# Optimization experiments

Hardware: AMD Instinct MI355X
Metric: run time of the kernel (lower is better)

The kernel has to match this reference:

```python
import jax, jax.numpy as jnp
import numpy as np

N_ATOMS = 60000
N_BONDS = 150000
MAX_NB = 6
N_MOLS = 2000
ATOM_FDIM = 133
BOND_FDIM = 14
HID = 300
DEPTH = 3
TAB = 16
FFN_HID = 300
FFN_IN = HID * 2 + TAB  # 616


def setup_inputs() -> dict:
    key = jax.random.key(0)
    ks = iter(jax.random.split(key, 40))
    d = {}
    for c in ("il", "hl"):
        d[f"f_atoms_{c}"] = jax.random.normal(next(ks), (N_ATOMS, ATOM_FDIM), jnp.float32)
        d[f"f_bonds_{c}"] = jax.random.normal(next(ks), (N_BONDS, BOND_FDIM), jnp.float32)
        d[f"a2b_{c}"] = jax.random.randint(next(ks), (N_ATOMS, MAX_NB), 0, N_BONDS, jnp.int32)
        d[f"b2a_{c}"] = jax.random.randint(next(ks), (N_BONDS,), 0, N_ATOMS, jnp.int32)
        d[f"b2revb_{c}"] = jax.random.randint(next(ks), (N_BONDS,), 0, N_BONDS, jnp.int32)
        d[f"mol_ids_{c}"] = jnp.sort(jax.random.randint(next(ks), (N_ATOMS,), 0, N_MOLS, jnp.int32))
        d[f"W_i_{c}"] = jax.random.normal(next(ks), (ATOM_FDIM + BOND_FDIM, HID), jnp.float32) * 0.05
        d[f"W_h_{c}"] = jax.random.normal(next(ks), (HID, HID), jnp.float32) * 0.05
        d[f"W_o_w_{c}"] = jax.random.normal(next(ks), (ATOM_FDIM + HID, HID), jnp.float32) * 0.05
        d[f"W_o_b_{c}"] = jax.random.normal(next(ks), (HID,), jnp.float32) * 0.05
    d["tabular"] = jax.random.normal(next(ks), (N_MOLS, TAB), jnp.float32)
    d["ffn_w1"] = jax.random.normal(next(ks), (FFN_IN, FFN_HID), jnp.float32) * 0.05
    d["ffn_b1"] = jax.random.normal(next(ks), (FFN_HID,), jnp.float32) * 0.05
    d["ffn_w2"] = jax.random.normal(next(ks), (FFN_HID, FFN_HID), jnp.float32) * 0.05
    d["ffn_b2"] = jax.random.normal(next(ks), (FFN_HID,), jnp.float32) * 0.05
    d["head_w"] = jax.random.normal(next(ks), (FFN_HID, 1), jnp.float32) * 0.05
    d["head_b"] = jax.random.normal(next(ks), (1,), jnp.float32) * 0.05
    return d


def _encode(f_atoms, f_bonds, a2b, b2a, b2revb, mol_ids, W_i, W_h, W_o_w, W_o_b):
    relu = jax.nn.relu
    # message init from [src atom feats, bond feats]
    msg = relu(jnp.concatenate([f_atoms[b2a], f_bonds], axis=1) @ W_i)  # [n_bonds, H]

    def step(m, _):
        nei = m[a2b].sum(axis=1)          # [n_atoms, H] gather-sum over incoming bonds
        nm = nei[b2a] - m[b2revb]         # exclude reverse bond
        return relu(nm @ W_h), None

    msg, _ = jax.lax.scan(step, msg, None, length=DEPTH - 1)
    a_msg = msg[a2b].sum(axis=1)          # [n_atoms, H]
    atom_h = relu(jnp.concatenate([f_atoms, a_msg], axis=1) @ W_o_w + W_o_b)
    sums = jax.ops.segment_sum(atom_h, mol_ids, num_segments=N_MOLS)
    cnt = jax.ops.segment_sum(jnp.ones((atom_h.shape[0],), atom_h.dtype), mol_ids, num_segments=N_MOLS)
    return sums / jnp.maximum(cnt, 1.0)[:, None]  # mean; zeros if empty mol


def reference(f_atoms_il, f_bonds_il, a2b_il, b2a_il, b2revb_il, mol_ids_il,
              W_i_il, W_h_il, W_o_w_il, W_o_b_il,
              f_atoms_hl, f_bonds_hl, a2b_hl, b2a_hl, b2revb_hl, mol_ids_hl,
              W_i_hl, W_h_hl, W_o_w_hl, W_o_b_hl,
              tabular, ffn_w1, ffn_b1, ffn_w2, ffn_b2, head_w, head_b):
    mv_il = _encode(f_atoms_il, f_bonds_il, a2b_il, b2a_il, b2revb_il, mol_ids_il,
                    W_i_il, W_h_il, W_o_w_il, W_o_b_il)
    mv_hl = _encode(f_atoms_hl, f_bonds_hl, a2b_hl, b2a_hl, b2revb_hl, mol_ids_hl,
                    W_i_hl, W_h_hl, W_o_w_hl, W_o_b_hl)
    combined = jnp.concatenate([mv_il, mv_hl, tabular], axis=1)  # [n_mols, 616]
    h = jax.nn.relu(combined @ ffn_w1 + ffn_b1)
    fp = jax.nn.relu(h @ ffn_w2 + ffn_b2)
    return fp @ head_w + head_b  # [n_mols, 1]
```

## Files before the change

kernel.cpp:

```cpp
#include <hip/hip_runtime.h>
#include <hip/hip_bf16.h>

#define N_ATOMS 60000
#define N_BONDS 150000
#define MAX_NB 6
#define N_MOLS 2000
#define ATOM_FDIM 133
#define BOND_FDIM 14
#define HID 300
#define TAB 16

typedef __hip_bfloat16 bf16;
typedef __attribute__((ext_vector_type(8))) short short8;
typedef __attribute__((ext_vector_type(4))) float f32x4;

__device__ __forceinline__ float b2f(short s) {
  return __uint_as_float(((unsigned int)(unsigned short)s) << 16);
}
__device__ __forceinline__ short f2b(float f) {
  bf16 h = __float2bfloat16(f);
  return __builtin_bit_cast(short, h);
}

__device__ __forceinline__ float ldv(const float* __restrict__ p, size_t i) { return p[i]; }
__device__ __forceinline__ float ldv(const bf16* __restrict__ p, size_t i) { return __bfloat162float(p[i]); }
__device__ __forceinline__ void stv(float* __restrict__ p, size_t i, float v) { p[i] = v; }
__device__ __forceinline__ void stv(bf16* __restrict__ p, size_t i, float v) { p[i] = __float2bfloat16(v); }


template<int AMODE>
__device__ __forceinline__ short8 fetchA(int row, int kg,
                                         const bf16* __restrict__ src0,
                                         const bf16* __restrict__ src1,
                                         const int* __restrict__ gidx) {
  if constexpr (AMODE == 0) {
    return *(const short8*)(src0 + (size_t)row * 320 + kg * 8);
  } else if constexpr (AMODE == 1) {
    if (kg < 18) {
      const int a = gidx[row];
      return *(const short8*)(src0 + (size_t)a * 144 + kg * 8);
    } else {
      return *(const short8*)(src1 + (size_t)row * 16 + (kg - 18) * 8);
    }
  } else {
    if (kg < 18) return *(const short8*)(src0 + (size_t)row * 144 + kg * 8);
    else if (kg < 58) return *(const short8*)(src1 + (size_t)row * 320 + (kg - 18) * 8);
    else { short8 z = {}; return z; }
  }
}

template<int AMODE, typename TO, int KSTEPS>
__global__ __launch_bounds__(256)
void mfma_gemm(const bf16* __restrict__ src0, const bf16* __restrict__ src1,
               const int* __restrict__ gidx, const bf16* __restrict__ Wt,
               const float* __restrict__ bias, TO* __restrict__ C,
               int M, int Ncols, int ostride) {
  __shared__ __align__(16) short As[128 * 32];
  __shared__ __align__(16) short Bs[64 * 32];
  const int t = threadIdx.x;
  const int bm = blockIdx.x * 128;
  const int bn = blockIdx.y * 64;
  const int w = t >> 6, lane = t & 63;
  const int wr = w >> 1, wc = w & 1;
  const int lr = lane & 15, lk = lane >> 4;
  f32x4 acc[4][2] = {};
  for (int kt = 0; kt < KSTEPS; ++kt) {
    #pragma unroll
    for (int i = 0; i < 2; ++i) {
      const int s = t + 256 * i;
      const int row = s >> 2, kgl = s & 3;
      const int grow = bm + row;
      short8 v = {};
      if (grow < M) v = fetchA<AMODE>(grow, kt * 4 + kgl, src0, src1, gidx);
      *(short8*)(As + row * 32 + ((kgl ^ (row & 3)) << 3)) = v;
    }
    {
      const int col = t >> 2, kgl = t & 3;
      short8 v = *(const short8*)(Wt + (size_t)(bn + col) * (KSTEPS * 32) + (size_t)(kt * 4 + kgl) * 8);
      *(short8*)(Bs + col * 32 + ((kgl ^ (col & 3)) << 3)) = v;
    }
    __syncthreads();
    short8 afr[4], bfr[2];
    #pragma unroll
    for (int m = 0; m < 4; ++m) {
      const int r = wr * 64 + m * 16 + lr;
      afr[m] = *(const short8*)(As + r * 32 + ((lk ^ (r & 3)) << 3));
    }
    #pragma unroll
    for (int n = 0; n < 2; ++n) {
      const int cc = wc * 32 + n * 16 + lr;
      bfr[n] = *(const short8*)(Bs + cc * 32 + ((lk ^ (cc & 3)) << 3));
    }
    #pragma unroll
    for (int m = 0; m < 4; ++m)
      #pragma unroll
      for (int n = 0; n < 2; ++n)
        acc[m][n] = __builtin_amdgcn_mfma_f32_16x16x32_bf16(afr[m], bfr[n], acc[m][n], 0, 0, 0);
    __syncthreads();
  }
  #pragma unroll
  for (int m = 0; m < 4; ++m) {
    #pragma unroll
    for (int n = 0; n < 2; ++n) {
      #pragma unroll
      for (int r = 0; r < 4; ++r) {
        const int row = bm + wr * 64 + m * 16 + lk * 4 + r;
        const int col = bn + wc * 32 + n * 16 + lr;
        if (row >= M) continue;
        if (col < Ncols) {
          float v = acc[m][n][r];
          if (bias) v += bias[col];
          stv(C, (size_t)row * ostride + col, fmaxf(v, 0.f));
        } else if (col < ostride) {
          stv(C, (size_t)row * ostride + col, 0.f);
        }
      }
    }
  }
}

__global__ __launch_bounds__(256)
void cvt_pad_kernel(const float* __restrict__ src, bf16* __restrict__ dst,
                    int rows, int scols, int dcols) {
  const int i = blockIdx.x * blockDim.x + threadIdx.x;
  if (i >= rows * dcols) return;
  const int r = i / dcols, c = i % dcols;
  dst[(size_t)r * dcols + c] = __float2bfloat16(c < scols ? src[(size_t)r * scols + c] : 0.f);
}

__global__ __launch_bounds__(256)
void wt_fill_kernel(const float* __restrict__ W, bf16* __restrict__ Wt,
                    int N, int Kp, int seg0_len, int seg1_dst, int seg1_src, int seg1_len) {
  const int i = blockIdx.x * blockDim.x + threadIdx.x;
  if (i >= 320 * Kp) return;
  const int n = i / Kp, kd = i % Kp;
  float v = 0.f;
  if (n < N) {
    if (kd < seg0_len) v = W[(size_t)kd * N + n];
    else if (kd >= seg1_dst && kd < seg1_dst + seg1_len)
      v = W[(size_t)(seg1_src + kd - seg1_dst) * N + n];
  }
  Wt[(size_t)n * Kp + kd] = __float2bfloat16(v);
}

__global__ __launch_bounds__(256)
void nei_sum16_kernel(const bf16* __restrict__ msg, const int* __restrict__ a2b,
                      bf16* __restrict__ nei) {
  const int i = blockIdx.x * blockDim.x + threadIdx.x;
  if (i >= N_ATOMS * 40) return;
  const int a = i / 40, c8 = (i % 40) * 8;
  const int* ab = a2b + (size_t)a * MAX_NB;
  float s[8] = {};
  #pragma unroll
  for (int j = 0; j < MAX_NB; ++j) {
    short8 v = *(const short8*)(msg + (size_t)ab[j] * 320 + c8);
    #pragma unroll
    for (int e = 0; e < 8; ++e) s[e] += b2f(v[e]);
  }
  short8 o;
  #pragma unroll
  for (int e = 0; e < 8; ++e) o[e] = f2b(s[e]);
  *(short8*)(nei + (size_t)a * 320 + c8) = o;
}

__global__ __launch_bounds__(256)
void nm16_kernel(const bf16* __restrict__ nei, const bf16* __restrict__ msg,
                 const int* __restrict__ b2a, const int* __restrict__ b2revb,
                 bf16* __restrict__ nm) {
  const int i = blockIdx.x * blockDim.x + threadIdx.x;
  if (i >= N_BONDS * 40) return;
  const int e = i / 40, c8 = (i % 40) * 8;
  const int a = b2a[e], r = b2revb[e];
  short8 u = *(const short8*)(nei + (size_t)a * 320 + c8);
  short8 v = *(const short8*)(msg + (size_t)r * 320 + c8);
  short8 o;
  #pragma unroll
  for (int k = 0; k < 8; ++k) o[k] = f2b(b2f(u[k]) - b2f(v[k]));
  *(short8*)(nm + (size_t)e * 320 + c8) = o;
}

template<int MODE, typename TA>
__device__ __forceinline__ float loadA(int row, int k,
                                       const TA* __restrict__ A,
                                       const int* __restrict__ idx,
                                       const float* __restrict__ aux0,
                                       const TA* __restrict__ aux1,
                                       const float* __restrict__ aux2,
                                       int K) {
  if constexpr (MODE == 0) {
    return ldv(A, (size_t)row * K + k);
  } else if constexpr (MODE == 1) {
    return (k < ATOM_FDIM) ? aux0[(size_t)idx[row] * ATOM_FDIM + k]
                           : aux2[(size_t)row * BOND_FDIM + (k - ATOM_FDIM)];
  } else if constexpr (MODE == 2) {
    return (k < ATOM_FDIM) ? aux0[(size_t)row * ATOM_FDIM + k]
                           : ldv(aux1, (size_t)row * HID + (k - ATOM_FDIM));
  } else {
    return (k < HID) ? aux0[(size_t)row * HID + k]
         : (k < 2 * HID) ? ldv(aux1, (size_t)row * HID + (k - HID))
         : aux2[(size_t)row * TAB + (k - 2 * HID)];
  }
}

constexpr int BM = 128, BN = 64, BK = 16;

template<int MODE, typename TA, typename TO>
__global__ __launch_bounds__(256)
void gemm_kernel(const TA* __restrict__ A, const int* __restrict__ idx,
                 const float* __restrict__ aux0, const TA* __restrict__ aux1,
                 const float* __restrict__ aux2,
                 const float* __restrict__ W, const float* __restrict__ bias,
                 TO* __restrict__ C, int M, int N, int K) {
  __shared__ float As[BK][BM + 4];
  __shared__ float Bs[BK][BN + 4];
  const int t = threadIdx.x;
  const int bm = blockIdx.x * BM;
  const int bn = blockIdx.y * BN;
  const int tx = t & 15;
  const int ty = t >> 4;
  float acc[8][4] = {};
  const int kTiles = (K + BK - 1) / BK;
  for (int kt = 0; kt < kTiles; ++kt) {
    const int k0 = kt * BK;
    {
      const int kk = t & 15;
      const int r0 = t >> 4;
      const int k = k0 + kk;
      #pragma unroll
      for (int i = 0; i < 8; ++i) {
        const int r = r0 + i * 16;
        const int row = bm + r;
        float v = 0.f;
        if (row < M && k < K) v = loadA<MODE, TA>(row, k, A, idx, aux0, aux1, aux2, K);
        As[kk][r] = v;
      }
    }
    {
      const int col = t & 63;
      const int kr = t >> 6;
      #pragma unroll
      for (int i = 0; i < 4; ++i) {
        const int k = k0 + kr + i * 4;
        float v = 0.f;
        if (k < K && (bn + col) < N) v = W[(size_t)k * N + bn + col];
        Bs[kr + i * 4][col] = v;
      }
    }
    __syncthreads();
    #pragma unroll
    for (int k = 0; k < BK; ++k) {
      float a[8], b[4];
      #pragma unroll
      for (int i = 0; i < 8; ++i) a[i] = As[k][ty * 8 + i];
      #pragma unroll
      for (int j = 0; j < 4; ++j) b[j] = Bs[k][tx * 4 + j];
      #pragma unroll
      for (int i = 0; i < 8; ++i)
        #pragma unroll
        for (int j = 0; j < 4; ++j)
          acc[i][j] = fmaf(a[i], b[j], acc[i][j]);
    }
    __syncthreads();
  }
  #pragma unroll
  for (int i = 0; i < 8; ++i) {
    const int row = bm + ty * 8 + i;
    if (row >= M) continue;
    #pragma unroll
    for (int j = 0; j < 4; ++j) {
      const int col = bn + tx * 4 + j;
      if (col >= N) continue;
      float v = acc[i][j];
      if (bias) v += bias[col];
      stv(C, (size_t)row * N + col, fmaxf(v, 0.f));
    }
  }
}

template<typename T>
__global__ __launch_bounds__(256)
void nei_sum_kernel(const T* __restrict__ msg, const int* __restrict__ a2b,
                    T* __restrict__ nei, int n_atoms) {
  const int i = blockIdx.x * blockDim.x + threadIdx.x;
  const int total = n_atoms * (HID / 4);
  if (i >= total) return;
  const int a = i / (HID / 4), c = (i % (HID / 4)) * 4;
  const int* ab = a2b + (size_t)a * MAX_NB;
  float s0 = 0.f, s1 = 0.f, s2 = 0.f, s3 = 0.f;
  #pragma unroll
  for (int j = 0; j < MAX_NB; ++j) {
    const size_t base = (size_t)ab[j] * HID + c;
    s0 += ldv(msg, base + 0); s1 += ldv(msg, base + 1);
    s2 += ldv(msg, base + 2); s3 += ldv(msg, base + 3);
  }
  const size_t ob = (size_t)a * HID + c;
  stv(nei, ob + 0, s0); stv(nei, ob + 1, s1);
  stv(nei, ob + 2, s2); stv(nei, ob + 3, s3);
}

template<typename T>
__global__ __launch_bounds__(256)
void nm_kernel(const T* __restrict__ nei, const T* __restrict__ msg,
               const int* __restrict__ b2a, const int* __restrict__ b2revb,
               T* __restrict__ nm, int n_bonds) {
  const int i = blockIdx.x * blockDim.x + threadIdx.x;
  const int total = n_bonds * (HID / 4);
  if (i >= total) return;
  const int e = i / (HID / 4), c = (i % (HID / 4)) * 4;
  const int a = b2a[e], r = b2revb[e];
  const size_t ub = (size_t)a * HID + c;
  const size_t vb = (size_t)r * HID + c;
  const size_t ob = (size_t)e * HID + c;
  stv(nm, ob + 0, ldv(nei, ub + 0) - ldv(msg, vb + 0));
  stv(nm, ob + 1, ldv(nei, ub + 1) - ldv(msg, vb + 1));
  stv(nm, ob + 2, ldv(nei, ub + 2) - ldv(msg, vb + 2));
  stv(nm, ob + 3, ldv(nei, ub + 3) - ldv(msg, vb + 3));
}

__device__ __forceinline__ int lower_bound_i(const int* __restrict__ arr, int n, int key) {
  int lo = 0, hi = n;
  while (lo < hi) { int mid = (lo + hi) >> 1; if (arr[mid] < key) lo = mid + 1; else hi = mid; }
  return lo;
}

__global__ __launch_bounds__(320)
void mol_mean_kernel(const float* __restrict__ atom_h, const int* __restrict__ mol_ids,
                     float* __restrict__ mv, int n_atoms) {
  const int m = blockIdx.x;
  const int start = lower_bound_i(mol_ids, n_atoms, m);
  const int end = lower_bound_i(mol_ids, n_atoms, m + 1);
  const int t = threadIdx.x;
  if (t < HID) {
    float s = 0.f;
    for (int a = start; a < end; ++a) s += atom_h[(size_t)a * HID + t];
    const float cnt = (float)(end - start);
    mv[(size_t)m * HID + t] = s / fmaxf(cnt, 1.0f);
  }
}

__global__ __launch_bounds__(256)
void head_kernel(const float* __restrict__ fp, const float* __restrict__ w,
                 const float* __restrict__ b, float* __restrict__ out, int n) {
  const int wid = (blockIdx.x * blockDim.x + threadIdx.x) >> 6;
  const int lane = threadIdx.x & 63;
  if (wid >= n) return;
  float s = 0.f;
  for (int k = lane; k < HID; k += 64) s += fp[(size_t)wid * HID + k] * w[k];
  #pragma unroll
  for (int off = 32; off; off >>= 1) s += __shfl_down(s, off, 64);
  if (lane == 0) out[wid] = s + b[0];
}

template<typename T>
static void run_encoder(const float* fa, const float* fb, const int* a2b,
                        const int* b2a, const int* b2revb, const int* mol_ids,
                        const float* W_i, const float* W_h,
                        const float* W_o_w, const float* W_o_b,
                        T* msgA, T* nmBuf, T* nei, float* atom_h, float* mv,
                        hipStream_t stream) {
  const dim3 blk(256);
  const dim3 gB((N_BONDS + BM - 1) / BM, (HID + BN - 1) / BN);
  const dim3 gA((N_ATOMS + BM - 1) / BM, (HID + BN - 1) / BN);
  const int neiBlocks = (N_ATOMS * (HID / 4) + 255) / 256;
  const int nmBlocks  = (N_BONDS * (HID / 4) + 255) / 256;

  gemm_kernel<1, T, T><<<gB, blk, 0, stream>>>((const T*)nullptr, b2a, fa, (const T*)nullptr, fb,
                                               W_i, nullptr, msgA,
                                               N_BONDS, HID, ATOM_FDIM + BOND_FDIM);
  for (int s = 0; s < 2; ++s) {
    nei_sum_kernel<T><<<neiBlocks, blk, 0, stream>>>(msgA, a2b, nei, N_ATOMS);
    nm_kernel<T><<<nmBlocks, blk, 0, stream>>>(nei, msgA, b2a, b2revb, nmBuf, N_BONDS);
    gemm_kernel<0, T, T><<<gB, blk, 0, stream>>>(nmBuf, nullptr, nullptr, (const T*)nullptr, nullptr,
                                                 W_h, nullptr, msgA,
                                                 N_BONDS, HID, HID);
  }
  nei_sum_kernel<T><<<neiBlocks, blk, 0, stream>>>(msgA, a2b, nei, N_ATOMS);
  gemm_kernel<2, T, float><<<gA, blk, 0, stream>>>((const T*)nullptr, nullptr, fa, nei, nullptr,
                                                   W_o_w, W_o_b, atom_h,
                                                   N_ATOMS, HID, ATOM_FDIM + HID);
  mol_mean_kernel<<<N_MOLS, 320, 0, stream>>>(atom_h, mol_ids, mv, N_ATOMS);
}

extern "C" void kernel_launch(void* const* d_in, const int* in_sizes, int n_in,
                              void* d_out, int out_size, void* d_ws, size_t ws_size,
                              hipStream_t stream) {
  const dim3 blk(256);

  const size_t msgBytes = (size_t)N_BONDS * 320 * 2;
  const size_t neiBytes = (size_t)N_ATOMS * 320 * 2;
  const size_t wtBytes  = (size_t)(320 * 160 + 320 * 320 + 320 * 480) * 2;
  const size_t mvBytes  = (size_t)4 * N_MOLS * HID * 4;
  const size_t needMFMA = 2 * msgBytes + neiBytes + wtBytes + mvBytes;

  const size_t nMsg = (size_t)N_BONDS * HID;
  const size_t nNei = (size_t)N_ATOMS * HID;
  const size_t nMol = (size_t)N_MOLS * HID;
  const size_t needSmall = (2 * nMsg + nNei) * sizeof(bf16) + 4 * nMol * sizeof(float);

  const float* tab     = (const float*)d_in[20];
  const float* ffn_w1  = (const float*)d_in[21];
  const float* ffn_b1  = (const float*)d_in[22];
  const float* ffn_w2  = (const float*)d_in[23];
  const float* ffn_b2  = (const float*)d_in[24];
  const float* head_w  = (const float*)d_in[25];
  const float* head_b  = (const float*)d_in[26];

  float *mv_il, *mv_hl, *h1, *fpb;

  if (ws_size >= needMFMA) {
    char* base = (char*)d_ws;
    bf16* msgA = (bf16*)base;
    bf16* msgB = (bf16*)(base + msgBytes);
    bf16* nei  = (bf16*)(base + 2 * msgBytes);
    bf16* WiT  = (bf16*)(base + 2 * msgBytes + neiBytes);
    bf16* WhT  = WiT + 320 * 160;
    bf16* WoT  = WhT + 320 * 320;
    float* mvf = (float*)(base + 2 * msgBytes + neiBytes + wtBytes);
    mv_il = mvf; mv_hl = mvf + nMol; h1 = mvf + 2 * nMol; fpb = mvf + 3 * nMol;
    bf16* fa16 = msgB;
    bf16* fb16 = msgB + (size_t)N_ATOMS * 144;
    float* atom_h = (float*)msgA;

    const dim3 gB((N_BONDS + 127) / 128, 5);
    const dim3 gA((N_ATOMS + 127) / 128, 5);
    const int neiBlk = (N_ATOMS * 40 + 255) / 256;
    const int nmBlk  = (N_BONDS * 40 + 255) / 256;

    for (int c = 0; c < 2; ++c) {
      const float* fa      = (const float*)d_in[c * 10 + 0];
      const float* fb      = (const float*)d_in[c * 10 + 1];
      const int*   a2b     = (const int*)d_in[c * 10 + 2];
      const int*   b2a     = (const int*)d_in[c * 10 + 3];
      const int*   b2revb  = (const int*)d_in[c * 10 + 4];
      const int*   mol_ids = (const int*)d_in[c * 10 + 5];
      const float* W_i     = (const float*)d_in[c * 10 + 6];
      const float* W_h     = (const float*)d_in[c * 10 + 7];
      const float* W_o_w   = (const float*)d_in[c * 10 + 8];
      const float* W_o_b   = (const float*)d_in[c * 10 + 9];
      float* mv = (c == 0) ? mv_il : mv_hl;

      cvt_pad_kernel<<<(N_ATOMS * 144 + 255) / 256, blk, 0, stream>>>(fa, fa16, N_ATOMS, 133, 144);
      cvt_pad_kernel<<<(N_BONDS * 16 + 255) / 256, blk, 0, stream>>>(fb, fb16, N_BONDS, 14, 16);
      wt_fill_kernel<<<(320 * 160 + 255) / 256, blk, 0, stream>>>(W_i, WiT, 300, 160, 133, 144, 133, 14);
      wt_fill_kernel<<<(320 * 320 + 255) / 256, blk, 0, stream>>>(W_h, WhT, 300, 320, 300, 0, 0, 0);
      wt_fill_kernel<<<(320 * 480 + 255) / 256, blk, 0, stream>>>(W_o_w, WoT, 300, 480, 133, 144, 133, 300);

      mfma_gemm<1, bf16, 5><<<gB, blk, 0, stream>>>(fa16, fb16, b2a, WiT, nullptr,
                                                    msgA, N_BONDS, 300, 320);
      for (int s = 0; s < 2; ++s) {
        nei_sum16_kernel<<<neiBlk, blk, 0, stream>>>(msgA, a2b, nei);
        nm16_kernel<<<nmBlk, blk, 0, stream>>>(nei, msgA, b2a, b2revb, msgB);
        mfma_gemm<0, bf16, 10><<<gB, blk, 0, stream>>>(msgB, nullptr, nullptr, WhT, nullptr,
                                                       msgA, N_BONDS, 300, 320);
      }
      cvt_pad_kernel<<<(N_ATOMS * 144 + 255) / 256, blk, 0, stream>>>(fa, fa16, N_ATOMS, 133, 144);
      nei_sum16_kernel<<<neiBlk, blk, 0, stream>>>(msgA, a2b, nei);
      mfma_gemm<2, float, 15><<<gA, blk, 0, stream>>>(fa16, nei, nullptr, WoT, W_o_b,
                                                      atom_h, N_ATOMS, 300, 300);
      mol_mean_kernel<<<N_MOLS, 320, 0, stream>>>(atom_h, mol_ids, mv, N_ATOMS);
    }
  } else if (ws_size >= needSmall) {
    bf16* p = (bf16*)d_ws;
    bf16* msgA_b = p;  p += nMsg;
    bf16* nm_b   = p;  p += nMsg;
    bf16* nei_b  = p;  p += nNei;
    float* q = (float*)p;
    mv_il = q; q += nMol;  mv_hl = q; q += nMol;
    h1 = q;    q += nMol;  fpb = q;
    float* atom_h = (float*)nm_b;

    for (int c = 0; c < 2; ++c) {
      const float* fa      = (const float*)d_in[c * 10 + 0];
      const float* fb      = (const float*)d_in[c * 10 + 1];
      const int*   a2b     = (const int*)d_in[c * 10 + 2];
      const int*   b2a     = (const int*)d_in[c * 10 + 3];
      const int*   b2revb  = (const int*)d_in[c * 10 + 4];
      const int*   mol_ids = (const int*)d_in[c * 10 + 5];
      const float* W_i     = (const float*)d_in[c * 10 + 6];
      const float* W_h     = (const float*)d_in[c * 10 + 7];
      const float* W_o_w   = (const float*)d_in[c * 10 + 8];
      const float* W_o_b   = (const float*)d_in[c * 10 + 9];
      float* mv = (c == 0) ? mv_il : mv_hl;
      run_encoder<bf16>(fa, fb, a2b, b2a, b2revb, mol_ids, W_i, W_h, W_o_w, W_o_b,
                        msgA_b, nm_b, nei_b, atom_h, mv, stream);
    }
  } else {
    hipMemsetAsync(d_out, 0, (size_t)out_size * sizeof(float), stream);
    return;
  }

  const dim3 gM((N_MOLS + BM - 1) / BM, (HID + BN - 1) / BN);
  gemm_kernel<3, float, float><<<gM, blk, 0, stream>>>(nullptr, nullptr, mv_il, mv_hl, tab,
                                                       ffn_w1, ffn_b1, h1,
                                                       N_MOLS, HID, 2 * HID + TAB);
  gemm_kernel<0, float, float><<<gM, blk, 0, stream>>>(h1, nullptr, nullptr, nullptr, nullptr,
                                                       ffn_w2, ffn_b2, fpb,
                                                       N_MOLS, HID, HID);
  head_kernel<<<(N_MOLS * 64 + 255) / 256, blk, 0, stream>>>(fpb, head_w, head_b,
                                                             (float*)d_out, N_MOLS);
}
```

Baseline: 1.698 ms.

## Fuse reverse-bond subtraction into message GEMM and fuse FFN head into one kernel

The nm16 kernel is removed. The GEMM A-tile loader (new AMODE 3) now gathers nei[b2a] and msg[b2revb] and subtracts them on the fly, so the intermediate nm buffer is no longer written and reread in each message-passing step. The two ping-pong buffers alternate between steps. The three-kernel FFN/head tail is replaced by a per-molecule fused kernel that computes both dense layers and the head dot product in shared memory. This cuts launches and intermediate traffic. The trade-off is extra gather work repeated inside the GEMM (once for each of the 5 column blocks), and a per-molecule FFN that rereads the weights for each of the 2000 blocks.

```diff
diff --git a/kernel.cpp b/kernel.cpp
--- a/kernel.cpp
+++ b/kernel.cpp
@@ -32,27 +32,36 @@
 __device__ __forceinline__ short8 fetchA(int row, int kg,
                                          const bf16* __restrict__ src0,
                                          const bf16* __restrict__ src1,
-                                         const int* __restrict__ gidx) {
-  if constexpr (AMODE == 0) {
-    return *(const short8*)(src0 + (size_t)row * 320 + kg * 8);
-  } else if constexpr (AMODE == 1) {
+                                         const int* __restrict__ gidx,
+                                         const int* __restrict__ gidx2) {
+  if constexpr (AMODE == 1) {
     if (kg < 18) {
       const int a = gidx[row];
       return *(const short8*)(src0 + (size_t)a * 144 + kg * 8);
     } else {
       return *(const short8*)(src1 + (size_t)row * 16 + (kg - 18) * 8);
     }
-  } else {
+  } else if constexpr (AMODE == 2) {
     if (kg < 18) return *(const short8*)(src0 + (size_t)row * 144 + kg * 8);
     else if (kg < 58) return *(const short8*)(src1 + (size_t)row * 320 + (kg - 18) * 8);
     else { short8 z = {}; return z; }
+  } else {
+    const int a = gidx[row];
+    const int r = gidx2[row];
+    short8 u = *(const short8*)(src0 + (size_t)a * 320 + kg * 8);
+    short8 v = *(const short8*)(src1 + (size_t)r * 320 + kg * 8);
+    short8 o;
+    #pragma unroll
+    for (int e = 0; e < 8; ++e) o[e] = f2b(b2f(u[e]) - b2f(v[e]));
+    return o;
   }
 }
 
 template<int AMODE, typename TO, int KSTEPS>
 __global__ __launch_bounds__(256)
 void mfma_gemm(const bf16* __restrict__ src0, const bf16* __restrict__ src1,
-               const int* __restrict__ gidx, const bf16* __restrict__ Wt,
+               const int* __restrict__ gidx, const int* __restrict__ gidx2,
+               const bf16* __restrict__ Wt,
                const float* __restrict__ bias, TO* __restrict__ C,
                int M, int Ncols, int ostride) {
   __shared__ __align__(16) short As[128 * 32];
@@ -71,7 +80,7 @@
       const int row = s >> 2, kgl = s & 3;
       const int grow = bm + row;
       short8 v = {};
-      if (grow < M) v = fetchA<AMODE>(grow, kt * 4 + kgl, src0, src1, gidx);
+      if (grow < M) v = fetchA<AMODE>(grow, kt * 4 + kgl, src0, src1, gidx, gidx2);
       *(short8*)(As + row * 32 + ((kgl ^ (row & 3)) << 3)) = v;
     }
     {
@@ -163,20 +172,45 @@
   *(short8*)(nei + (size_t)a * 320 + c8) = o;
 }
 
-__global__ __launch_bounds__(256)
-void nm16_kernel(const bf16* __restrict__ nei, const bf16* __restrict__ msg,
-                 const int* __restrict__ b2a, const int* __restrict__ b2revb,
-                 bf16* __restrict__ nm) {
-  const int i = blockIdx.x * blockDim.x + threadIdx.x;
-  if (i >= N_BONDS * 40) return;
-  const int e = i / 40, c8 = (i % 40) * 8;
-  const int a = b2a[e], r = b2revb[e];
-  short8 u = *(const short8*)(nei + (size_t)a * 320 + c8);
-  short8 v = *(const short8*)(msg + (size_t)r * 320 + c8);
-  short8 o;
-  #pragma unroll
-  for (int k = 0; k < 8; ++k) o[k] = f2b(b2f(u[k]) - b2f(v[k]));
-  *(short8*)(nm + (size_t)e * 320 + c8) = o;
+__global__ __launch_bounds__(320)
+void ffn_fused_kernel(const float* __restrict__ mv_il, const float* __restrict__ mv_hl,
+                      const float* __restrict__ tab,
+                      const float* __restrict__ w1, const float* __restrict__ b1,
+                      const float* __restrict__ w2, const float* __restrict__ b2,
+                      const float* __restrict__ hw, const float* __restrict__ hb,
+                      float* __restrict__ out) {
+  __shared__ float comb[616];
+  __shared__ float h[300];
+  __shared__ float fp[304];
+  const int m = blockIdx.x;
+  const int t = threadIdx.x;
+  for (int k = t; k < 616; k += 320) {
+    float v;
+    if (k < 300) v = mv_il[(size_t)m * 300 + k];
+    else if (k < 600) v = mv_hl[(size_t)m * 300 + (k - 300)];
+    else v = tab[(size_t)m * TAB + (k - 600)];
+    comb[k] = v;
+  }
+  __syncthreads();
+  if (t < 300) {
+    float a = 0.f;
+    for (int k = 0; k < 616; ++k) a = fmaf(comb[k], w1[(size_t)k * 300 + t], a);
+    h[t] = fmaxf(a + b1[t], 0.f);
+  }
+  __syncthreads();
+  if (t < 300) {
+    float a = 0.f;
+    for (int k = 0; k < 300; ++k) a = fmaf(h[k], w2[(size_t)k * 300 + t], a);
+    fp[t] = fmaxf(a + b2[t], 0.f) * hw[t];
+  }
+  __syncthreads();
+  if (t < 64) {
+    float s = 0.f;
+    for (int k = t; k < 300; k += 64) s += fp[k];
+    #pragma unroll
+    for (int off = 32; off; off >>= 1) s += __shfl_down(s, off, 64);
+    if (t == 0) out[m] = s + hb[0];
+  }
 }
 
 template<int MODE, typename TA>
@@ -192,13 +226,9 @@
   } else if constexpr (MODE == 1) {
     return (k < ATOM_FDIM) ? aux0[(size_t)idx[row] * ATOM_FDIM + k]
                            : aux2[(size_t)row * BOND_FDIM + (k - ATOM_FDIM)];
-  } else if constexpr (MODE == 2) {
+  } else {
     return (k < ATOM_FDIM) ? aux0[(size_t)row * ATOM_FDIM + k]
                            : ldv(aux1, (size_t)row * HID + (k - ATOM_FDIM));
-  } else {
-    return (k < HID) ? aux0[(size_t)row * HID + k]
-         : (k < 2 * HID) ? ldv(aux1, (size_t)row * HID + (k - HID))
-         : aux2[(size_t)row * TAB + (k - 2 * HID)];
   }
 }
 
@@ -338,19 +368,6 @@
   }
 }
 
-__global__ __launch_bounds__(256)
-void head_kernel(const float* __restrict__ fp, const float* __restrict__ w,
-                 const float* __restrict__ b, float* __restrict__ out, int n) {
-  const int wid = (blockIdx.x * blockDim.x + threadIdx.x) >> 6;
-  const int lane = threadIdx.x & 63;
-  if (wid >= n) return;
-  float s = 0.f;
-  for (int k = lane; k < HID; k += 64) s += fp[(size_t)wid * HID + k] * w[k];
-  #pragma unroll
-  for (int off = 32; off; off >>= 1) s += __shfl_down(s, off, 64);
-  if (lane == 0) out[wid] = s + b[0];
-}
-
 template<typename T>
 static void run_encoder(const float* fa, const float* fb, const int* a2b,
                         const int* b2a, const int* b2revb, const int* mol_ids,
@@ -405,7 +422,7 @@
   const float* head_w  = (const float*)d_in[25];
   const float* head_b  = (const float*)d_in[26];
 
-  float *mv_il, *mv_hl, *h1, *fpb;
+  float *mv_il, *mv_hl;
 
   if (ws_size >= needMFMA) {
     char* base = (char*)d_ws;
@@ -416,7 +433,7 @@
     bf16* WhT  = WiT + 320 * 160;
     bf16* WoT  = WhT + 320 * 320;
     float* mvf = (float*)(base + 2 * msgBytes + neiBytes + wtBytes);
-    mv_il = mvf; mv_hl = mvf + nMol; h1 = mvf + 2 * nMol; fpb = mvf + 3 * nMol;
+    mv_il = mvf; mv_hl = mvf + nMol;
     bf16* fa16 = msgB;
     bf16* fb16 = msgB + (size_t)N_ATOMS * 144;
     float* atom_h = (float*)msgA;
@@ -424,7 +441,6 @@
     const dim3 gB((N_BONDS + 127) / 128, 5);
     const dim3 gA((N_ATOMS + 127) / 128, 5);
     const int neiBlk = (N_ATOMS * 40 + 255) / 256;
-    const int nmBlk  = (N_BONDS * 40 + 255) / 256;
 
     for (int c = 0; c < 2; ++c) {
       const float* fa      = (const float*)d_in[c * 10 + 0];
@@ -445,17 +461,17 @@
       wt_fill_kernel<<<(320 * 320 + 255) / 256, blk, 0, stream>>>(W_h, WhT, 300, 320, 300, 0, 0, 0);
       wt_fill_kernel<<<(320 * 480 + 255) / 256, blk, 0, stream>>>(W_o_w, WoT, 300, 480, 133, 144, 133, 300);
 
-      mfma_gemm<1, bf16, 5><<<gB, blk, 0, stream>>>(fa16, fb16, b2a, WiT, nullptr,
+      mfma_gemm<1, bf16, 5><<<gB, blk, 0, stream>>>(fa16, fb16, b2a, nullptr, WiT, nullptr,
                                                     msgA, N_BONDS, 300, 320);
-      for (int s = 0; s < 2; ++s) {
-        nei_sum16_kernel<<<neiBlk, blk, 0, stream>>>(msgA, a2b, nei);
-        nm16_kernel<<<nmBlk, blk, 0, stream>>>(nei, msgA, b2a, b2revb, msgB);
-        mfma_gemm<0, bf16, 10><<<gB, blk, 0, stream>>>(msgB, nullptr, nullptr, WhT, nullptr,
-                                                       msgA, N_BONDS, 300, 320);
-      }
+      nei_sum16_kernel<<<neiBlk, blk, 0, stream>>>(msgA, a2b, nei);
+      mfma_gemm<3, bf16, 10><<<gB, blk, 0, stream>>>(nei, msgA, b2a, b2revb, WhT, nullptr,
+                                                     msgB, N_BONDS, 300, 320);
+      nei_sum16_kernel<<<neiBlk, blk, 0, stream>>>(msgB, a2b, nei);
+      mfma_gemm<3, bf16, 10><<<gB, blk, 0, stream>>>(nei, msgB, b2a, b2revb, WhT, nullptr,
+                                                     msgA, N_BONDS, 300, 320);
+      nei_sum16_kernel<<<neiBlk, blk, 0, stream>>>(msgA, a2b, nei);
       cvt_pad_kernel<<<(N_ATOMS * 144 + 255) / 256, blk, 0, stream>>>(fa, fa16, N_ATOMS, 133, 144);
-      nei_sum16_kernel<<<neiBlk, blk, 0, stream>>>(msgA, a2b, nei);
-      mfma_gemm<2, float, 15><<<gA, blk, 0, stream>>>(fa16, nei, nullptr, WoT, W_o_b,
+      mfma_gemm<2, float, 15><<<gA, blk, 0, stream>>>(fa16, nei, nullptr, nullptr, WoT, W_o_b,
                                                       atom_h, N_ATOMS, 300, 300);
       mol_mean_kernel<<<N_MOLS, 320, 0, stream>>>(atom_h, mol_ids, mv, N_ATOMS);
     }
@@ -465,8 +481,7 @@
     bf16* nm_b   = p;  p += nMsg;
     bf16* nei_b  = p;  p += nNei;
     float* q = (float*)p;
-    mv_il = q; q += nMol;  mv_hl = q; q += nMol;
-    h1 = q;    q += nMol;  fpb = q;
+    mv_il = q; q += nMol;  mv_hl = q;
     float* atom_h = (float*)nm_b;
 
     for (int c = 0; c < 2; ++c) {
@@ -489,13 +504,7 @@
     return;
   }
 
-  const dim3 gM((N_MOLS + BM - 1) / BM, (HID + BN - 1) / BN);
-  gemm_kernel<3, float, float><<<gM, blk, 0, stream>>>(nullptr, nullptr, mv_il, mv_hl, tab,
-                                                       ffn_w1, ffn_b1, h1,
-                                                       N_MOLS, HID, 2 * HID + TAB);
-  gemm_kernel<0, float, float><<<gM, blk, 0, stream>>>(h1, nullptr, nullptr, nullptr, nullptr,
-                                                       ffn_w2, ffn_b2, fpb,
-                                                       N_MOLS, HID, HID);
-  head_kernel<<<(N_MOLS * 64 + 255) / 256, blk, 0, stream>>>(fpb, head_w, head_b,
-                                                             (float*)d_out, N_MOLS);
-}
+  ffn_fused_kernel<<<N_MOLS, 320, 0, stream>>>(mv_il, mv_hl, tab,
+                                               ffn_w1, ffn_b1, ffn_w2, ffn_b2,
+                                               head_w, head_b, (float*)d_out);
+}
```

New measurement: 1.929 ms. 1.14x slower.
